# Performance work log

Hardware: AMD Instinct MI355X
Metric: run time of the kernel (lower is better)

## Reference

```python
import jax, jax.numpy as jnp
import numpy as np

N_S = 50000
N_T = 50000
E = 1600000
IN_C = 128
HID_C = 128
OUT_C = 64


def _sage_conv(x_src, x_dst, edge_index, W_l, W_r, b, n_dst):
    """PyG bipartite SAGEConv, aggr='mean': lin_l(mean_j x_src[j]) + lin_r(x_dst).
    lin_l has bias, lin_r does not."""
    row, col = edge_index[0], edge_index[1]
    msg = x_src[row]                                          # [E, F_in] gather
    summed = jax.ops.segment_sum(msg, col, num_segments=n_dst)  # [n_dst, F_in]
    cnt = jax.ops.segment_sum(jnp.ones((row.shape[0],), x_src.dtype), col,
                              num_segments=n_dst)
    mean = summed / jnp.maximum(cnt, 1.0)[:, None]            # zero for isolated nodes
    return mean @ W_l + b + x_dst @ W_r


def setup_inputs() -> dict:
    key = jax.random.key(0)
    ks = jax.random.split(key, 20)
    x_s = jax.random.normal(ks[0], (N_S, IN_C), dtype=jnp.float32)
    x_t = jax.random.normal(ks[1], (N_T, IN_C), dtype=jnp.float32)
    s2t = jnp.stack([jax.random.randint(ks[2], (E,), 0, N_S),
                     jax.random.randint(ks[3], (E,), 0, N_T)])
    t2s = jnp.stack([jax.random.randint(ks[4], (E,), 0, N_T),
                     jax.random.randint(ks[5], (E,), 0, N_S)])

    def lin(k, fi, fo):
        return jax.random.normal(k, (fi, fo), dtype=jnp.float32) / np.sqrt(fi)

    return {
        'x_s': x_s, 'x_t': x_t, 's2t': s2t, 't2s': t2s,
        'W1s_l': lin(ks[6], IN_C, HID_C), 'W1s_r': lin(ks[7], IN_C, HID_C),
        'b1s': jnp.zeros((HID_C,), jnp.float32),
        'W1t_l': lin(ks[8], IN_C, HID_C), 'W1t_r': lin(ks[9], IN_C, HID_C),
        'b1t': jnp.zeros((HID_C,), jnp.float32),
        'W2s_l': lin(ks[10], HID_C, OUT_C), 'W2s_r': lin(ks[11], HID_C, OUT_C),
        'b2s': jnp.zeros((OUT_C,), jnp.float32),
        'W2t_l': lin(ks[12], HID_C, OUT_C), 'W2t_r': lin(ks[13], HID_C, OUT_C),
        'b2t': jnp.zeros((OUT_C,), jnp.float32),
    }


def reference(x_s, x_t, s2t, t2s,
              W1s_l, W1s_r, b1s, W1t_l, W1t_r, b1t,
              W2s_l, W2s_r, b2s, W2t_l, W2t_r, b2t):
    # layer 1 (cross-side message passing)
    x_new_s = _sage_conv(x_t, x_s, t2s, W1s_l, W1s_r, b1s, N_S)
    x_new_t = _sage_conv(x_s, x_t, s2t, W1t_l, W1t_r, b1t, N_T)
    # layer 2
    z_s = _sage_conv(x_new_t, x_new_s, t2s, W2s_l, W2s_r, b2s, N_S)
    z_t = _sage_conv(x_new_s, x_new_t, s2t, W2t_l, W2t_r, b2t, N_T)
    return (z_s, z_t)
```

## Files before the change

### kernel.cpp

```cpp
#include <hip/hip_runtime.h>

typedef unsigned int u32;
typedef unsigned short u16;
typedef __attribute__((ext_vector_type(4))) float f32x4;
typedef __attribute__((ext_vector_type(2))) float f32x2;
typedef __attribute__((ext_vector_type(8))) short bf16x8;

static inline int cdiv(int a, int b) { return (a + b - 1) / b; }

#define NBKT 512
#define BSHIFT 7
#define BNODES 128
#define EPB2 8192
#define CAP 5120

__device__ inline u32 pk_bf16(float a, float b) {
  u32 ua = __builtin_bit_cast(u32, a);
  ua += 0x7fffu + ((ua >> 16) & 1u);
  u32 ub = __builtin_bit_cast(u32, b);
  ub += 0x7fffu + ((ub >> 16) & 1u);
  return (ua >> 16) | (ub & 0xffff0000u);
}

__global__ __launch_bounds__(256) void cvt_in_k(const float* __restrict__ xs,
                                                const float* __restrict__ xt,
                                                int n4S, int n4T,
                                                uint2* __restrict__ xsbf,
                                                uint2* __restrict__ xtbf,
                                                u32* __restrict__ xsf8,
                                                u32* __restrict__ xtf8) {
  int i = blockIdx.x * 256 + threadIdx.x;
  const float* src;
  uint2* obf;
  u32* of8;
  int q;
  if (i < n4S) {
    src = xs; obf = xsbf; of8 = xsf8; q = i;
  } else {
    q = i - n4S;
    if (q >= n4T) return;
    src = xt; obf = xtbf; of8 = xtf8;
  }
  float4 v = *reinterpret_cast<const float4*>(src + (size_t)q * 4);
  uint2 b;
  b.x = pk_bf16(v.x, v.y);
  b.y = pk_bf16(v.z, v.w);
  obf[q] = b;
  u32 p = 0;
  p = __builtin_amdgcn_cvt_pk_fp8_f32(v.x, v.y, p, false);
  p = __builtin_amdgcn_cvt_pk_fp8_f32(v.z, v.w, p, true);
  of8[q] = p;
}

__global__ __launch_bounds__(256) void cvtW_k(const float* __restrict__ W1sl,
                                              const float* __restrict__ W1sr,
                                              const float* __restrict__ W1tl,
                                              const float* __restrict__ W1tr,
                                              const float* __restrict__ W2A_s,
                                              const float* __restrict__ W2B_s,
                                              const float* __restrict__ W2A_t,
                                              const float* __restrict__ W2B_t,
                                              u16* __restrict__ out) {
  int seg = blockIdx.x * 256 + threadIdx.x;
  if (seg >= 12288) return;
  const float* W;
  int ncol, base, local;
  if (seg < 8192) {
    int m = seg >> 11; local = seg & 2047; ncol = 128; base = m * 16384;
    W = m == 0 ? W1sl : m == 1 ? W1sr : m == 2 ? W1tl : W1tr;
  } else {
    int m = (seg - 8192) >> 10; local = (seg - 8192) & 1023; ncol = 64; base = 65536 + m * 8192;
    W = m == 0 ? W2A_s : m == 1 ? W2B_s : m == 2 ? W2A_t : W2B_t;
  }
  int col = local >> 4;
  int k0 = (local & 15) * 8;
  u16 tmp[8];
#pragma unroll
  for (int e = 0; e < 8; ++e) {
    float v = W[(size_t)(k0 + e) * ncol + col];
    tmp[e] = (u16)(pk_bf16(v, 0.f) & 0xffffu);
  }
  *reinterpret_cast<uint4*>(out + (size_t)base + col * 128 + k0) =
      *reinterpret_cast<uint4*>(tmp);
}


__global__ __launch_bounds__(512) void scatfuse2_k(const int* __restrict__ rowS,
                                                   const int* __restrict__ colS,
                                                   const int* __restrict__ rowT,
                                                   const int* __restrict__ colT,
                                                   int E, int nblk,
                                                   int* __restrict__ gcur,
                                                   u32* __restrict__ bktS,
                                                   u32* __restrict__ bktT) {
  __shared__ u32 stage[EPB2];
  __shared__ int h[NBKT], lstart[NBKT], lpos[NBKT], gbase[NBKT];
  int b = blockIdx.x;
  const int *row, *col;
  u32* bkt;
  int* gc;
  if (b < nblk) {
    row = rowS; col = colS; bkt = bktS; gc = gcur;
  } else {
    b -= nblk; row = rowT; col = colT; bkt = bktT; gc = gcur + NBKT;
  }
  int t = threadIdx.x;
  h[t] = 0;
  __syncthreads();
  int base = b * EPB2, end = min(base + EPB2, E);
  for (int i = base + t; i < end; i += 512) atomicAdd(&h[col[i] >> BSHIFT], 1);
  __syncthreads();
  lstart[t] = h[t];
  __syncthreads();
  for (int off = 1; off < NBKT; off <<= 1) {
    int x = (t >= off) ? lstart[t - off] : 0;
    __syncthreads();
    if (t >= off) lstart[t] += x;
    __syncthreads();
  }
  {
    int hc = h[t];
    int ls = lstart[t] - hc;
    lstart[t] = ls;
    lpos[t] = ls;
    gbase[t] = hc ? atomicAdd(&gc[t], hc) : 0;
  }
  __syncthreads();
  for (int i = base + t; i < end; i += 512) {
    int c = col[i];
    int p = atomicAdd(&lpos[c >> BSHIFT], 1);
    stage[p] = ((u32)row[i] << 16) | (u32)c;
  }
  __syncthreads();
  int total = end - base;
  for (int j = t; j < total; j += 512) {
    u32 v = stage[j];
    u32 d = v & 0xffffu;
    int bi = d >> BSHIFT;
    int gp = gbase[bi] + (j - lstart[bi]);
    bkt[(size_t)bi * CAP + gp] = ((v >> 16) << BSHIFT) | (d & (BNODES - 1));
  }
}


__global__ __launch_bounds__(256) void sortb_k(u32* __restrict__ bktS,
                                               u32* __restrict__ bktT,
                                               const int* __restrict__ gcur,
                                               int NS, int NT,
                                               u32* __restrict__ stdegS,
                                               u32* __restrict__ stdegT) {
  __shared__ u32 srcs[CAP];
  __shared__ int cnt[BNODES], excl[BNODES], st[BNODES], cur[BNODES];
  int nbkS = (NS + BNODES - 1) >> BSHIFT;
  int b = blockIdx.x;
  u32 *bkt, *stdeg;
  int N, ec;
  if (b < nbkS) {
    bkt = bktS + (size_t)b * CAP; ec = gcur[b]; stdeg = stdegS; N = NS;
  } else {
    b -= nbkS;
    bkt = bktT + (size_t)b * CAP; ec = gcur[NBKT + b]; stdeg = stdegT; N = NT;
  }
  int node0 = b << BSHIFT;
  int t = threadIdx.x;
  if (t < BNODES) cnt[t] = 0;
  __syncthreads();
  for (int i = t; i < ec; i += 256) atomicAdd(&cnt[bkt[i] & (BNODES - 1)], 1);
  __syncthreads();
  if (t < BNODES) excl[t] = cnt[t];
  __syncthreads();
  for (int off = 1; off < BNODES; off <<= 1) {
    int x = 0;
    if (t < BNODES && t >= off) x = excl[t - off];
    __syncthreads();
    if (t < BNODES && t >= off) excl[t] += x;
    __syncthreads();
  }
  if (t < BNODES) {
    int s0 = excl[t] - cnt[t];
    st[t] = s0;
    cur[t] = s0;
  }
  __syncthreads();
  for (int i = t; i < ec; i += 256) {
    u32 p = bkt[i];
    int ps = atomicAdd(&cur[p & (BNODES - 1)], 1);
    srcs[ps] = p >> BSHIFT;
  }
  __syncthreads();
  for (int i = t; i < ec; i += 256) bkt[i] = srcs[i];
  if (t < BNODES) {
    int node = node0 + t;
    if (node < N) stdeg[node] = ((u32)st[t] << 16) | (u32)cnt[t];
  }
}


__global__ __launch_bounds__(256) void agg128D_k(const u32* __restrict__ xs_f8,
                                                 const u32* __restrict__ xt_f8,
                                                 const u32* __restrict__ bktS,
                                                 const u32* __restrict__ bktT,
                                                 const u32* __restrict__ stdegS,
                                                 const u32* __restrict__ stdegT,
                                                 int NS, int NT,
                                                 u32* __restrict__ mean_s,
                                                 u32* __restrict__ mean_t) {
  int nbS = (NS + 15) >> 4;
  int nbT = (NT + 15) >> 4;
  int slot = blockIdx.x & 7;
  int pair = blockIdx.x >> 3;
  int gid = threadIdx.x >> 4, fl = threadIdx.x & 15;
  const u32 *xf8, *bkt, *stdeg;
  u32* outm;
  int N, node;
  if (slot < 4) {
    int blk = pair * 4 + slot;
    if (blk >= nbS) return;
    xf8 = xt_f8; bkt = bktS; stdeg = stdegS; outm = mean_s; N = NS;
    node = blk * 16 + gid;
  } else {
    int blk = pair * 4 + (slot - 4);
    if (blk >= nbT) return;
    xf8 = xs_f8; bkt = bktT; stdeg = stdegT; outm = mean_t; N = NT;
    node = blk * 16 + gid;
  }
  if (node >= N) return;
  u32 sd = stdeg[node];
  int deg = (int)(sd & 0xffffu);
  const u32* csr = bkt + (size_t)(node >> BSHIFT) * CAP + (sd >> 16);
  f32x2 a0 = {0.f, 0.f}, a1 = {0.f, 0.f}, a2 = {0.f, 0.f}, a3 = {0.f, 0.f};
  int i = 0;
  for (; i + 8 <= deg; i += 8) {
    int c[8];
#pragma unroll
    for (int j = 0; j < 8; ++j) c[j] = csr[i + j];
    uint2 v[8];
#pragma unroll
    for (int j = 0; j < 8; ++j)
      v[j] = *reinterpret_cast<const uint2*>(xf8 + (size_t)c[j] * 32 + fl * 2);
#pragma unroll
    for (int j = 0; j < 8; ++j) {
      a0 += __builtin_amdgcn_cvt_pk_f32_fp8(v[j].x, false);
      a1 += __builtin_amdgcn_cvt_pk_f32_fp8(v[j].x, true);
      a2 += __builtin_amdgcn_cvt_pk_f32_fp8(v[j].y, false);
      a3 += __builtin_amdgcn_cvt_pk_f32_fp8(v[j].y, true);
    }
  }
  for (; i + 4 <= deg; i += 4) {
    int c[4];
#pragma unroll
    for (int j = 0; j < 4; ++j) c[j] = csr[i + j];
    uint2 v[4];
#pragma unroll
    for (int j = 0; j < 4; ++j)
      v[j] = *reinterpret_cast<const uint2*>(xf8 + (size_t)c[j] * 32 + fl * 2);
#pragma unroll
    for (int j = 0; j < 4; ++j) {
      a0 += __builtin_amdgcn_cvt_pk_f32_fp8(v[j].x, false);
      a1 += __builtin_amdgcn_cvt_pk_f32_fp8(v[j].x, true);
      a2 += __builtin_amdgcn_cvt_pk_f32_fp8(v[j].y, false);
      a3 += __builtin_amdgcn_cvt_pk_f32_fp8(v[j].y, true);
    }
  }
  for (; i < deg; ++i) {
    int c0 = csr[i];
    uint2 v0 = *reinterpret_cast<const uint2*>(xf8 + (size_t)c0 * 32 + fl * 2);
    a0 += __builtin_amdgcn_cvt_pk_f32_fp8(v0.x, false);
    a1 += __builtin_amdgcn_cvt_pk_f32_fp8(v0.x, true);
    a2 += __builtin_amdgcn_cvt_pk_f32_fp8(v0.y, false);
    a3 += __builtin_amdgcn_cvt_pk_f32_fp8(v0.y, true);
  }
  float inv = deg > 0 ? 1.f / (float)deg : 0.f;
  uint4 p;
  p.x = pk_bf16(a0.x * inv, a0.y * inv);
  p.y = pk_bf16(a1.x * inv, a1.y * inv);
  p.z = pk_bf16(a2.x * inv, a2.y * inv);
  p.w = pk_bf16(a3.x * inv, a3.y * inv);
  *reinterpret_cast<uint4*>(outm + (size_t)node * 64 + fl * 4) = p;
}


__global__ __launch_bounds__(256) void agg64D_k(const u32* __restrict__ hs_f8,
                                                const u32* __restrict__ ht_f8,
                                                const u32* __restrict__ bktS,
                                                const u32* __restrict__ bktT,
                                                const u32* __restrict__ stdegS,
                                                const u32* __restrict__ stdegT,
                                                int NS, int NT,
                                                const float* __restrict__ g_s,
                                                const float* __restrict__ g_t,
                                                const float* __restrict__ b2s,
                                                const float* __restrict__ b2t,
                                                float* __restrict__ z_s,
                                                float* __restrict__ z_t) {
  int nbS = (NS + 15) >> 4;
  int nbT = (NT + 15) >> 4;
  int slot = blockIdx.x & 7;
  int pair = blockIdx.x >> 3;
  int gid = threadIdx.x >> 4, fl = threadIdx.x & 15;
  const u32 *hf8, *bkt, *stdeg;
  const float *g, *bias;
  float* z;
  int N, node;
  if (slot < 4) {
    int blk = pair * 4 + slot;
    if (blk >= nbS) return;
    hf8 = ht_f8; bkt = bktS; stdeg = stdegS; g = g_s; bias = b2s; z = z_s; N = NS;
    node = blk * 16 + gid;
  } else {
    int blk = pair * 4 + (slot - 4);
    if (blk >= nbT) return;
    hf8 = hs_f8; bkt = bktT; stdeg = stdegT; g = g_t; bias = b2t; z = z_t; N = NT;
    node = blk * 16 + gid;
  }
  if (node >= N) return;
  u32 sd = stdeg[node];
  int deg = (int)(sd & 0xffffu);
  const u32* csr = bkt + (size_t)(node >> BSHIFT) * CAP + (sd >> 16);
  f32x2 a0 = {0.f, 0.f}, a1 = {0.f, 0.f};
  int i = 0;
  for (; i + 8 <= deg; i += 8) {
    int c[8];
#pragma unroll
    for (int j = 0; j < 8; ++j) c[j] = csr[i + j];
    u32 v[8];
#pragma unroll
    for (int j = 0; j < 8; ++j) v[j] = hf8[(size_t)c[j] * 16 + fl];
#pragma unroll
    for (int j = 0; j < 8; ++j) {
      a0 += __builtin_amdgcn_cvt_pk_f32_fp8(v[j], false);
      a1 += __builtin_amdgcn_cvt_pk_f32_fp8(v[j], true);
    }
  }
  for (; i + 4 <= deg; i += 4) {
    int c[4];
#pragma unroll
    for (int j = 0; j < 4; ++j) c[j] = csr[i + j];
    u32 v[4];
#pragma unroll
    for (int j = 0; j < 4; ++j) v[j] = hf8[(size_t)c[j] * 16 + fl];
#pragma unroll
    for (int j = 0; j < 4; ++j) {
      a0 += __builtin_amdgcn_cvt_pk_f32_fp8(v[j], false);
      a1 += __builtin_amdgcn_cvt_pk_f32_fp8(v[j], true);
    }
  }
  for (; i < deg; ++i) {
    u32 v0 = hf8[(size_t)csr[i] * 16 + fl];
    a0 += __builtin_amdgcn_cvt_pk_f32_fp8(v0, false);
    a1 += __builtin_amdgcn_cvt_pk_f32_fp8(v0, true);
  }
  float inv = deg > 0 ? 1.f / (float)deg : 0.f;
  float4 gv = *reinterpret_cast<const float4*>(g + (size_t)node * 64 + fl * 4);
  float4 bv = *reinterpret_cast<const float4*>(bias + fl * 4);
  float4 r;
  r.x = a0.x * inv + gv.x + bv.x;
  r.y = a0.y * inv + gv.y + bv.y;
  r.z = a1.x * inv + gv.z + bv.z;
  r.w = a1.y * inv + gv.w + bv.w;
  *reinterpret_cast<float4*>(z + (size_t)node * 64 + fl * 4) = r;
}


__global__ __launch_bounds__(256) void gemm1_dual_k(
    const u16* __restrict__ mean_s, const u16* __restrict__ xs_bf,
    const u16* __restrict__ mean_t, const u16* __restrict__ xt_bf,
    const u16* __restrict__ Wt_s0, const u16* __restrict__ Wt_s1,
    const u16* __restrict__ Wt_t0, const u16* __restrict__ Wt_t1,
    const float* __restrict__ b1s, const float* __restrict__ b1t,
    u16* __restrict__ xnew_s, u16* __restrict__ xnew_t, int NS, int NT) {
  int nb1 = (NS + 255) >> 8;
  int b = blockIdx.x;
  const u16 *A0, *A1, *Wt0, *Wt1;
  const float* bias;
  u16* out;
  int M, rowBase;
  if (b < nb1) {
    A0 = mean_s; A1 = xs_bf; Wt0 = Wt_s0; Wt1 = Wt_s1; bias = b1s; out = xnew_s;
    M = NS; rowBase = b * 256;
  } else {
    A0 = mean_t; A1 = xt_bf; Wt0 = Wt_t0; Wt1 = Wt_t1; bias = b1t; out = xnew_t;
    M = NT; rowBase = (b - nb1) * 256;
  }
  const int lane = threadIdx.x & 63;
  const int wid = threadIdx.x >> 6;
  const int r16 = lane & 15;
  const int kg = lane >> 4;
  rowBase += wid * 64;

  int r[4];
#pragma unroll
  for (int f = 0; f < 4; ++f) r[f] = min(rowBase + f * 16 + r16, M - 1);

#pragma unroll
  for (int cbh = 0; cbh < 2; ++cbh) {
    f32x4 acc[4][4];
#pragma unroll
    for (int f = 0; f < 4; ++f)
#pragma unroll
      for (int j = 0; j < 4; ++j) acc[f][j] = (f32x4){0.f, 0.f, 0.f, 0.f};

#pragma unroll
    for (int ch = 0; ch < 8; ++ch) {
      const u16* A = (ch < 4) ? A0 : A1;
      const u16* Wt = (ch < 4) ? Wt0 : Wt1;
      const int koff = (ch & 3) * 32 + kg * 8;
      bf16x8 x[4];
#pragma unroll
      for (int f = 0; f < 4; ++f)
        x[f] = *reinterpret_cast<const bf16x8*>(A + (size_t)r[f] * 128 + koff);
#pragma unroll
      for (int cb = 0; cb < 4; ++cb) {
        int cbg = cbh * 4 + cb;
        bf16x8 w = *reinterpret_cast<const bf16x8*>(Wt + (size_t)(cbg * 16 + r16) * 128 + koff);
#pragma unroll
        for (int f = 0; f < 4; ++f)
          acc[f][cb] = __builtin_amdgcn_mfma_f32_16x16x32_bf16(w, x[f], acc[f][cb], 0, 0, 0);
      }
    }

#pragma unroll
    for (int cb = 0; cb < 4; ++cb) {
      int cbg = cbh * 4 + cb;
      float4 bv = *reinterpret_cast<const float4*>(bias + cbg * 16 + kg * 4);
#pragma unroll
      for (int f = 0; f < 4; ++f) {
        int row = rowBase + f * 16 + r16;
        if (row < M) {
          f32x4 a = acc[f][cb];
          uint2 p;
          p.x = pk_bf16(a[0] + bv.x, a[1] + bv.y);
          p.y = pk_bf16(a[2] + bv.z, a[3] + bv.w);
          *reinterpret_cast<uint2*>(out + (size_t)row * 128 + cbg * 16 + kg * 4) = p;
        }
      }
    }
  }
}


__global__ __launch_bounds__(256) void gemm2_dual_k(
    const u16* __restrict__ xnew_s, const u16* __restrict__ xnew_t,
    const u16* __restrict__ WtA_s, const u16* __restrict__ WtB_s,
    const u16* __restrict__ WtA_t, const u16* __restrict__ WtB_t,
    u32* __restrict__ hs_f8, u32* __restrict__ ht_f8,
    float* __restrict__ g_s, float* __restrict__ g_t, int NS, int NT) {
  int nb1 = (NS + 255) >> 8;
  int b = blockIdx.x;
  const u16 *X, *WtA, *WtB;
  u32* h;
  float* g;
  int M, rowBase;
  if (b < nb1) {
    X = xnew_s; WtA = WtA_s; WtB = WtB_s; h = hs_f8; g = g_s; M = NS; rowBase = b * 256;
  } else {
    X = xnew_t; WtA = WtA_t; WtB = WtB_t; h = ht_f8; g = g_t; M = NT;
    rowBase = (b - nb1) * 256;
  }
  const int lane = threadIdx.x & 63;
  const int wid = threadIdx.x >> 6;
  const int r16 = lane & 15;
  const int kg = lane >> 4;
  rowBase += wid * 64;

  int r[4];
#pragma unroll
  for (int f = 0; f < 4; ++f) r[f] = min(rowBase + f * 16 + r16, M - 1);

#pragma unroll
  for (int cbh = 0; cbh < 2; ++cbh) {
    const u16* Wt = (cbh == 0) ? WtA : WtB;
    f32x4 acc[4][4];
#pragma unroll
    for (int f = 0; f < 4; ++f)
#pragma unroll
      for (int j = 0; j < 4; ++j) acc[f][j] = (f32x4){0.f, 0.f, 0.f, 0.f};

#pragma unroll
    for (int ch = 0; ch < 4; ++ch) {
      const int koff = ch * 32 + kg * 8;
      bf16x8 x[4];
#pragma unroll
      for (int f = 0; f < 4; ++f)
        x[f] = *reinterpret_cast<const bf16x8*>(X + (size_t)r[f] * 128 + koff);
#pragma unroll
      for (int cb = 0; cb < 4; ++cb) {
        bf16x8 w = *reinterpret_cast<const bf16x8*>(Wt + (size_t)(cb * 16 + r16) * 128 + koff);
#pragma unroll
        for (int f = 0; f < 4; ++f)
          acc[f][cb] = __builtin_amdgcn_mfma_f32_16x16x32_bf16(w, x[f], acc[f][cb], 0, 0, 0);
      }
    }

#pragma unroll
    for (int cb = 0; cb < 4; ++cb) {
#pragma unroll
      for (int f = 0; f < 4; ++f) {
        int row = rowBase + f * 16 + r16;
        if (row < M) {
          f32x4 a = acc[f][cb];
          if (cbh == 0) {
            u32 p = 0;
            p = __builtin_amdgcn_cvt_pk_fp8_f32(a[0], a[1], p, false);
            p = __builtin_amdgcn_cvt_pk_fp8_f32(a[2], a[3], p, true);
            h[(size_t)row * 16 + cb * 4 + kg] = p;
          } else {
            *reinterpret_cast<f32x4*>(g + (size_t)row * 64 + cb * 16 + kg * 4) = a;
          }
        }
      }
    }
  }
}


extern "C" void kernel_launch(void* const* d_in, const int* in_sizes, int n_in,
                              void* d_out, int out_size, void* d_ws, size_t ws_size,
                              hipStream_t stream) {
  const float* x_s = (const float*)d_in[0];
  const float* x_t = (const float*)d_in[1];
  const int* s2t = (const int*)d_in[2];
  const int* t2s = (const int*)d_in[3];
  const float* W1s_l = (const float*)d_in[4];
  const float* W1s_r = (const float*)d_in[5];
  const float* b1s = (const float*)d_in[6];
  const float* W1t_l = (const float*)d_in[7];
  const float* W1t_r = (const float*)d_in[8];
  const float* b1t = (const float*)d_in[9];
  const float* W2s_l = (const float*)d_in[10];
  const float* W2s_r = (const float*)d_in[11];
  const float* b2s = (const float*)d_in[12];
  const float* W2t_l = (const float*)d_in[13];
  const float* W2t_r = (const float*)d_in[14];
  const float* b2t = (const float*)d_in[15];

  const int NS = in_sizes[0] / 128;
  const int NT = in_sizes[1] / 128;
  const int E = in_sizes[2] / 2;

  char* ws = (char*)d_ws;
  size_t off = 0;
  auto alloc = [&](size_t bytes) -> void* {
    void* p = ws + off;
    off = (off + bytes + 255) & ~(size_t)255;
    return p;
  };

  const int nbkS = cdiv(NS, BNODES);
  const int nbkT = cdiv(NT, BNODES);
  const int nblk2 = cdiv(E, EPB2);

  int* gcur = (int*)alloc(2 * NBKT * 4);
  u16* Wt = (u16*)alloc(98304 * 2);
  u32* bktS = (u32*)alloc((size_t)nbkS * CAP * 4);
  u32* bktT = (u32*)alloc((size_t)nbkT * CAP * 4);
  u32* stdegS = (u32*)alloc((size_t)NS * 4);
  u32* stdegT = (u32*)alloc((size_t)NT * 4);

  char* R2 = (char*)alloc((size_t)(NS + NT) * 512);
  u16* xnew_s = (u16*)alloc((size_t)(NS + NT) * 256);
  u16* xnew_t = xnew_s + (size_t)NS * 128;
  u16* xs_bf = (u16*)alloc((size_t)(NS + NT) * 256);
  u16* xt_bf = xs_bf + (size_t)NS * 128;

  u16* mean_s = (u16*)R2;
  u16* mean_t = mean_s + (size_t)NS * 128;
  u32* hs_f8 = (u32*)R2;
  u32* ht_f8 = hs_f8 + (size_t)NS * 16;
  float* g_s = (float*)(ht_f8 + (size_t)NT * 16);
  float* g_t = g_s + (size_t)NS * 64;

  u32* xs_f8 = (u32*)(R2 + (size_t)(NS + NT) * 384);
  u32* xt_f8 = xs_f8 + (size_t)NS * 32;

  u16* Wt1s_l = Wt;
  u16* Wt1s_r = Wt + 16384;
  u16* Wt1t_l = Wt + 32768;
  u16* Wt1t_r = Wt + 49152;
  u16* Wt2A_s = Wt + 65536;
  u16* Wt2B_s = Wt + 73728;
  u16* Wt2A_t = Wt + 81920;
  u16* Wt2B_t = Wt + 90112;

  float* z_s = (float*)d_out;
  float* z_t = (float*)d_out + (size_t)NS * 64;

  cvt_in_k<<<cdiv(NS * 32 + NT * 32, 256), 256, 0, stream>>>(
      x_s, x_t, NS * 32, NT * 32, (uint2*)xs_bf, (uint2*)xt_bf, xs_f8, xt_f8);
  cvtW_k<<<48, 256, 0, stream>>>(W1s_l, W1s_r, W1t_l, W1t_r,
                                 W2t_l, W2s_r, W2s_l, W2t_r, Wt);
  hipMemsetAsync(gcur, 0, 2 * NBKT * 4, stream);

  scatfuse2_k<<<2 * nblk2, 512, 0, stream>>>(t2s, t2s + E, s2t, s2t + E, E, nblk2,
                                             gcur, bktS, bktT);
  sortb_k<<<nbkS + nbkT, 256, 0, stream>>>(bktS, bktT, gcur, NS, NT, stdegS, stdegT);

  const int npair128 = cdiv(max(cdiv(NS, 16), cdiv(NT, 16)), 4);

  agg128D_k<<<npair128 * 8, 256, 0, stream>>>(
      xs_f8, xt_f8, bktS, bktT, stdegS, stdegT, NS, NT, (u32*)mean_s, (u32*)mean_t);
  gemm1_dual_k<<<cdiv(NS, 256) + cdiv(NT, 256), 256, 0, stream>>>(
      mean_s, xs_bf, mean_t, xt_bf, Wt1s_l, Wt1s_r, Wt1t_l, Wt1t_r,
      b1s, b1t, xnew_s, xnew_t, NS, NT);

  gemm2_dual_k<<<cdiv(NS, 256) + cdiv(NT, 256), 256, 0, stream>>>(
      xnew_s, xnew_t, Wt2A_s, Wt2B_s, Wt2A_t, Wt2B_t, hs_f8, ht_f8, g_s, g_t, NS, NT);
  agg64D_k<<<npair128 * 8, 256, 0, stream>>>(
      hs_f8, ht_f8, bktS, bktT, stdegS, stdegT, NS, NT,
      g_s, g_t, b2s, b2t, z_s, z_t);
}
```

Before: 195.5 us.

## Fuse input/weight conversion into scatter kernel and prefetch CSR indices in aggregation

Merges the input conversion, the weight conversion and the edge bucket-scatter kernels into a single heterogeneous launch, with block ranges picking the role. This removes two launches and lets the independent conversion work overlap with the scatter. The aggregation loops now software-pipeline the loads of the next 8 neighbor indices while gathering the current ones, and the 4-wide remainder loop is dropped. Conversion blocks now carry the scatter kernel's large shared-memory allocation, which may lower their occupancy.

```diff
diff --git a/kernel.cpp b/kernel.cpp
--- a/kernel.cpp
+++ b/kernel.cpp
@@ -22,123 +22,118 @@
   return (ua >> 16) | (ub & 0xffff0000u);
 }
 
-__global__ __launch_bounds__(256) void cvt_in_k(const float* __restrict__ xs,
-                                                const float* __restrict__ xt,
-                                                int n4S, int n4T,
-                                                uint2* __restrict__ xsbf,
-                                                uint2* __restrict__ xtbf,
-                                                u32* __restrict__ xsf8,
-                                                u32* __restrict__ xtf8) {
-  int i = blockIdx.x * 256 + threadIdx.x;
-  const float* src;
-  uint2* obf;
-  u32* of8;
-  int q;
-  if (i < n4S) {
-    src = xs; obf = xsbf; of8 = xsf8; q = i;
-  } else {
-    q = i - n4S;
-    if (q >= n4T) return;
-    src = xt; obf = xtbf; of8 = xtf8;
-  }
-  float4 v = *reinterpret_cast<const float4*>(src + (size_t)q * 4);
-  uint2 b;
-  b.x = pk_bf16(v.x, v.y);
-  b.y = pk_bf16(v.z, v.w);
-  obf[q] = b;
-  u32 p = 0;
-  p = __builtin_amdgcn_cvt_pk_fp8_f32(v.x, v.y, p, false);
-  p = __builtin_amdgcn_cvt_pk_fp8_f32(v.z, v.w, p, true);
-  of8[q] = p;
-}
-
-__global__ __launch_bounds__(256) void cvtW_k(const float* __restrict__ W1sl,
-                                              const float* __restrict__ W1sr,
-                                              const float* __restrict__ W1tl,
-                                              const float* __restrict__ W1tr,
-                                              const float* __restrict__ W2A_s,
-                                              const float* __restrict__ W2B_s,
-                                              const float* __restrict__ W2A_t,
-                                              const float* __restrict__ W2B_t,
-                                              u16* __restrict__ out) {
-  int seg = blockIdx.x * 256 + threadIdx.x;
-  if (seg >= 12288) return;
-  const float* W;
-  int ncol, base, local;
-  if (seg < 8192) {
-    int m = seg >> 11; local = seg & 2047; ncol = 128; base = m * 16384;
-    W = m == 0 ? W1sl : m == 1 ? W1sr : m == 2 ? W1tl : W1tr;
-  } else {
-    int m = (seg - 8192) >> 10; local = (seg - 8192) & 1023; ncol = 64; base = 65536 + m * 8192;
-    W = m == 0 ? W2A_s : m == 1 ? W2B_s : m == 2 ? W2A_t : W2B_t;
-  }
-  int col = local >> 4;
-  int k0 = (local & 15) * 8;
-  u16 tmp[8];
-#pragma unroll
-  for (int e = 0; e < 8; ++e) {
-    float v = W[(size_t)(k0 + e) * ncol + col];
-    tmp[e] = (u16)(pk_bf16(v, 0.f) & 0xffffu);
-  }
-  *reinterpret_cast<uint4*>(out + (size_t)base + col * 128 + k0) =
-      *reinterpret_cast<uint4*>(tmp);
-}
-
-
-__global__ __launch_bounds__(512) void scatfuse2_k(const int* __restrict__ rowS,
-                                                   const int* __restrict__ colS,
-                                                   const int* __restrict__ rowT,
-                                                   const int* __restrict__ colT,
-                                                   int E, int nblk,
-                                                   int* __restrict__ gcur,
-                                                   u32* __restrict__ bktS,
-                                                   u32* __restrict__ bktT) {
+
+__global__ __launch_bounds__(512) void prep_k(
+    const int* __restrict__ rowS, const int* __restrict__ colS,
+    const int* __restrict__ rowT, const int* __restrict__ colT,
+    int E, int nblk, int* __restrict__ gcur,
+    u32* __restrict__ bktS, u32* __restrict__ bktT,
+    const float* __restrict__ xs, const float* __restrict__ xt,
+    int n4S, int n4T,
+    uint2* __restrict__ xsbf, uint2* __restrict__ xtbf,
+    u32* __restrict__ xsf8, u32* __restrict__ xtf8,
+    const float* __restrict__ W1sl, const float* __restrict__ W1sr,
+    const float* __restrict__ W1tl, const float* __restrict__ W1tr,
+    const float* __restrict__ W2A_s, const float* __restrict__ W2B_s,
+    const float* __restrict__ W2A_t, const float* __restrict__ W2B_t,
+    u16* __restrict__ Wout, int ncvt) {
   __shared__ u32 stage[EPB2];
   __shared__ int h[NBKT], lstart[NBKT], lpos[NBKT], gbase[NBKT];
   int b = blockIdx.x;
-  const int *row, *col;
-  u32* bkt;
-  int* gc;
-  if (b < nblk) {
-    row = rowS; col = colS; bkt = bktS; gc = gcur;
+  int t = threadIdx.x;
+
+  if (b < 2 * nblk) {
+    const int *row, *col;
+    u32* bkt;
+    int* gc;
+    if (b < nblk) {
+      row = rowS; col = colS; bkt = bktS; gc = gcur;
+    } else {
+      b -= nblk; row = rowT; col = colT; bkt = bktT; gc = gcur + NBKT;
+    }
+    h[t] = 0;
+    __syncthreads();
+    int base = b * EPB2, end = min(base + EPB2, E);
+    for (int i = base + t; i < end; i += 512) atomicAdd(&h[col[i] >> BSHIFT], 1);
+    __syncthreads();
+    lstart[t] = h[t];
+    __syncthreads();
+    for (int off = 1; off < NBKT; off <<= 1) {
+      int x = (t >= off) ? lstart[t - off] : 0;
+      __syncthreads();
+      if (t >= off) lstart[t] += x;
+      __syncthreads();
+    }
+    {
+      int hc = h[t];
+      int ls = lstart[t] - hc;
+      lstart[t] = ls;
+      lpos[t] = ls;
+      gbase[t] = hc ? atomicAdd(&gc[t], hc) : 0;
+    }
+    __syncthreads();
+    for (int i = base + t; i < end; i += 512) {
+      int c = col[i];
+      int p = atomicAdd(&lpos[c >> BSHIFT], 1);
+      stage[p] = ((u32)row[i] << 16) | (u32)c;
+    }
+    __syncthreads();
+    int total = end - base;
+    for (int j = t; j < total; j += 512) {
+      u32 v = stage[j];
+      u32 d = v & 0xffffu;
+      int bi = d >> BSHIFT;
+      int gp = gbase[bi] + (j - lstart[bi]);
+      bkt[(size_t)bi * CAP + gp] = ((v >> 16) << BSHIFT) | (d & (BNODES - 1));
+    }
+  } else if (b < 2 * nblk + ncvt) {
+    int bb = b - 2 * nblk;
+#pragma unroll
+    for (int k = 0; k < 4; ++k) {
+      int q = (bb * 4 + k) * 512 + t;
+      if (q >= n4S + n4T) break;
+      const float* src;
+      uint2* obf;
+      u32* of8;
+      int qq;
+      if (q < n4S) {
+        src = xs; obf = xsbf; of8 = xsf8; qq = q;
+      } else {
+        src = xt; obf = xtbf; of8 = xtf8; qq = q - n4S;
+      }
+      float4 v = *reinterpret_cast<const float4*>(src + (size_t)qq * 4);
+      uint2 bw;
+      bw.x = pk_bf16(v.x, v.y);
+      bw.y = pk_bf16(v.z, v.w);
+      obf[qq] = bw;
+      u32 p = 0;
+      p = __builtin_amdgcn_cvt_pk_fp8_f32(v.x, v.y, p, false);
+      p = __builtin_amdgcn_cvt_pk_fp8_f32(v.z, v.w, p, true);
+      of8[qq] = p;
+    }
   } else {
-    b -= nblk; row = rowT; col = colT; bkt = bktT; gc = gcur + NBKT;
-  }
-  int t = threadIdx.x;
-  h[t] = 0;
-  __syncthreads();
-  int base = b * EPB2, end = min(base + EPB2, E);
-  for (int i = base + t; i < end; i += 512) atomicAdd(&h[col[i] >> BSHIFT], 1);
-  __syncthreads();
-  lstart[t] = h[t];
-  __syncthreads();
-  for (int off = 1; off < NBKT; off <<= 1) {
-    int x = (t >= off) ? lstart[t - off] : 0;
-    __syncthreads();
-    if (t >= off) lstart[t] += x;
-    __syncthreads();
-  }
-  {
-    int hc = h[t];
-    int ls = lstart[t] - hc;
-    lstart[t] = ls;
-    lpos[t] = ls;
-    gbase[t] = hc ? atomicAdd(&gc[t], hc) : 0;
-  }
-  __syncthreads();
-  for (int i = base + t; i < end; i += 512) {
-    int c = col[i];
-    int p = atomicAdd(&lpos[c >> BSHIFT], 1);
-    stage[p] = ((u32)row[i] << 16) | (u32)c;
-  }
-  __syncthreads();
-  int total = end - base;
-  for (int j = t; j < total; j += 512) {
-    u32 v = stage[j];
-    u32 d = v & 0xffffu;
-    int bi = d >> BSHIFT;
-    int gp = gbase[bi] + (j - lstart[bi]);
-    bkt[(size_t)bi * CAP + gp] = ((v >> 16) << BSHIFT) | (d & (BNODES - 1));
+    int seg = (b - 2 * nblk - ncvt) * 512 + t;
+    if (seg >= 12288) return;
+    const float* W;
+    int ncol, base, local;
+    if (seg < 8192) {
+      int m = seg >> 11; local = seg & 2047; ncol = 128; base = m * 16384;
+      W = m == 0 ? W1sl : m == 1 ? W1sr : m == 2 ? W1tl : W1tr;
+    } else {
+      int m = (seg - 8192) >> 10; local = (seg - 8192) & 1023; ncol = 64;
+      base = 65536 + m * 8192;
+      W = m == 0 ? W2A_s : m == 1 ? W2B_s : m == 2 ? W2A_t : W2B_t;
+    }
+    int col = local >> 4;
+    int k0 = (local & 15) * 8;
+    u16 tmp[8];
+#pragma unroll
+    for (int e = 0; e < 8; ++e) {
+      float v = W[(size_t)(k0 + e) * ncol + col];
+      tmp[e] = (u16)(pk_bf16(v, 0.f) & 0xffffu);
+    }
+    *reinterpret_cast<uint4*>(Wout + (size_t)base + col * 128 + k0) =
+        *reinterpret_cast<uint4*>(tmp);
   }
 }
 
@@ -230,36 +225,33 @@
   const u32* csr = bkt + (size_t)(node >> BSHIFT) * CAP + (sd >> 16);
   f32x2 a0 = {0.f, 0.f}, a1 = {0.f, 0.f}, a2 = {0.f, 0.f}, a3 = {0.f, 0.f};
   int i = 0;
-  for (; i + 8 <= deg; i += 8) {
-    int c[8];
-#pragma unroll
-    for (int j = 0; j < 8; ++j) c[j] = csr[i + j];
-    uint2 v[8];
-#pragma unroll
-    for (int j = 0; j < 8; ++j)
-      v[j] = *reinterpret_cast<const uint2*>(xf8 + (size_t)c[j] * 32 + fl * 2);
-#pragma unroll
-    for (int j = 0; j < 8; ++j) {
-      a0 += __builtin_amdgcn_cvt_pk_f32_fp8(v[j].x, false);
-      a1 += __builtin_amdgcn_cvt_pk_f32_fp8(v[j].x, true);
-      a2 += __builtin_amdgcn_cvt_pk_f32_fp8(v[j].y, false);
-      a3 += __builtin_amdgcn_cvt_pk_f32_fp8(v[j].y, true);
-    }
-  }
-  for (; i + 4 <= deg; i += 4) {
-    int c[4];
-#pragma unroll
-    for (int j = 0; j < 4; ++j) c[j] = csr[i + j];
-    uint2 v[4];
-#pragma unroll
-    for (int j = 0; j < 4; ++j)
-      v[j] = *reinterpret_cast<const uint2*>(xf8 + (size_t)c[j] * 32 + fl * 2);
-#pragma unroll
-    for (int j = 0; j < 4; ++j) {
-      a0 += __builtin_amdgcn_cvt_pk_f32_fp8(v[j].x, false);
-      a1 += __builtin_amdgcn_cvt_pk_f32_fp8(v[j].x, true);
-      a2 += __builtin_amdgcn_cvt_pk_f32_fp8(v[j].y, false);
-      a3 += __builtin_amdgcn_cvt_pk_f32_fp8(v[j].y, true);
+  if (deg >= 8) {
+    int nc[8];
+#pragma unroll
+    for (int j = 0; j < 8; ++j) nc[j] = csr[j];
+    while (true) {
+      int c[8];
+#pragma unroll
+      for (int j = 0; j < 8; ++j) c[j] = nc[j];
+      int inext = i + 8;
+      bool more = (inext + 8 <= deg);
+      if (more) {
+#pragma unroll
+        for (int j = 0; j < 8; ++j) nc[j] = csr[inext + j];
+      }
+      uint2 v[8];
+#pragma unroll
+      for (int j = 0; j < 8; ++j)
+        v[j] = *reinterpret_cast<const uint2*>(xf8 + (size_t)c[j] * 32 + fl * 2);
+#pragma unroll
+      for (int j = 0; j < 8; ++j) {
+        a0 += __builtin_amdgcn_cvt_pk_f32_fp8(v[j].x, false);
+        a1 += __builtin_amdgcn_cvt_pk_f32_fp8(v[j].x, true);
+        a2 += __builtin_amdgcn_cvt_pk_f32_fp8(v[j].y, false);
+        a3 += __builtin_amdgcn_cvt_pk_f32_fp8(v[j].y, true);
+      }
+      i = inext;
+      if (!more) break;
     }
   }
   for (; i < deg; ++i) {
@@ -319,30 +311,30 @@
   const u32* csr = bkt + (size_t)(node >> BSHIFT) * CAP + (sd >> 16);
   f32x2 a0 = {0.f, 0.f}, a1 = {0.f, 0.f};
   int i = 0;
-  for (; i + 8 <= deg; i += 8) {
-    int c[8];
-#pragma unroll
-    for (int j = 0; j < 8; ++j) c[j] = csr[i + j];
-    u32 v[8];
-#pragma unroll
-    for (int j = 0; j < 8; ++j) v[j] = hf8[(size_t)c[j] * 16 + fl];
-#pragma unroll
-    for (int j = 0; j < 8; ++j) {
-      a0 += __builtin_amdgcn_cvt_pk_f32_fp8(v[j], false);
-      a1 += __builtin_amdgcn_cvt_pk_f32_fp8(v[j], true);
-    }
-  }
-  for (; i + 4 <= deg; i += 4) {
-    int c[4];
-#pragma unroll
-    for (int j = 0; j < 4; ++j) c[j] = csr[i + j];
-    u32 v[4];
-#pragma unroll
-    for (int j = 0; j < 4; ++j) v[j] = hf8[(size_t)c[j] * 16 + fl];
-#pragma unroll
-    for (int j = 0; j < 4; ++j) {
-      a0 += __builtin_amdgcn_cvt_pk_f32_fp8(v[j], false);
-      a1 += __builtin_amdgcn_cvt_pk_f32_fp8(v[j], true);
+  if (deg >= 8) {
+    int nc[8];
+#pragma unroll
+    for (int j = 0; j < 8; ++j) nc[j] = csr[j];
+    while (true) {
+      int c[8];
+#pragma unroll
+      for (int j = 0; j < 8; ++j) c[j] = nc[j];
+      int inext = i + 8;
+      bool more = (inext + 8 <= deg);
+      if (more) {
+#pragma unroll
+        for (int j = 0; j < 8; ++j) nc[j] = csr[inext + j];
+      }
+      u32 v[8];
+#pragma unroll
+      for (int j = 0; j < 8; ++j) v[j] = hf8[(size_t)c[j] * 16 + fl];
+#pragma unroll
+      for (int j = 0; j < 8; ++j) {
+        a0 += __builtin_amdgcn_cvt_pk_f32_fp8(v[j], false);
+        a1 += __builtin_amdgcn_cvt_pk_f32_fp8(v[j], true);
+      }
+      i = inext;
+      if (!more) break;
     }
   }
   for (; i < deg; ++i) {
@@ -585,14 +577,16 @@
   float* z_s = (float*)d_out;
   float* z_t = (float*)d_out + (size_t)NS * 64;
 
-  cvt_in_k<<<cdiv(NS * 32 + NT * 32, 256), 256, 0, stream>>>(
-      x_s, x_t, NS * 32, NT * 32, (uint2*)xs_bf, (uint2*)xt_bf, xs_f8, xt_f8);
-  cvtW_k<<<48, 256, 0, stream>>>(W1s_l, W1s_r, W1t_l, W1t_r,
-                                 W2t_l, W2s_r, W2s_l, W2t_r, Wt);
   hipMemsetAsync(gcur, 0, 2 * NBKT * 4, stream);
 
-  scatfuse2_k<<<2 * nblk2, 512, 0, stream>>>(t2s, t2s + E, s2t, s2t + E, E, nblk2,
-                                             gcur, bktS, bktT);
+  const int n4S = NS * 32, n4T = NT * 32;
+  const int ncvt = cdiv(n4S + n4T, 2048);
+  const int ncvtw = cdiv(12288, 512);
+  prep_k<<<2 * nblk2 + ncvt + ncvtw, 512, 0, stream>>>(
+      t2s, t2s + E, s2t, s2t + E, E, nblk2, gcur, bktS, bktT,
+      x_s, x_t, n4S, n4T, (uint2*)xs_bf, (uint2*)xt_bf, xs_f8, xt_f8,
+      W1s_l, W1s_r, W1t_l, W1t_r, W2t_l, W2s_r, W2s_l, W2t_r, Wt, ncvt);
+
   sortb_k<<<nbkS + nbkT, 256, 0, stream>>>(bktS, bktT, gcur, NS, NT, stdegS, stdegT);
 
   const int npair128 = cdiv(max(cdiv(NS, 16), cdiv(NT, 16)), 4);
```

New measurement: 200.7 us. +2.6%, slower.
